# Performance work log

Measured on AMD Instinct MI355X. Metric: run time of the kernel, lower is better.

## Reference

```python
import jax, jax.numpy as jnp
import numpy as np

B, C, L = 8, 512, 2048   # batch, input_dim (channels), sequence length
H = 8                    # multihead_cnt
K = 3                    # kernel_dim
DH = C // H              # per-head dim = 64
SCALE = 1.0 / float(np.sqrt(C))  # module divides by sqrt(input_dim), not sqrt(head_dim)


def _conv1d(x, w, b):
    # x: [B, C, L], w: [C_out, C_in, K], padding=1 keeps L
    y = jax.lax.conv_general_dilated(x, w, window_strides=(1,), padding=[(1, 1)],
                                     dimension_numbers=('NCH', 'OIH', 'NCH'))
    return y + b[None, :, None]


def setup_inputs() -> dict:
    key = jax.random.key(0)
    ks = jax.random.split(key, 7)
    x = jax.random.normal(ks[0], (B, C, L), dtype=jnp.float32)
    # xavier_normal_ std for Conv1d weight [C, C, K]: sqrt(2 / (fan_in + fan_out)), fan = C*K
    std = float(np.sqrt(2.0 / (C * K + C * K)))
    inp = {'x': x}
    for i in range(3):  # conv_cnt = 3 -> q, k, v convolutions
        inp[f'w{i}'] = jax.random.normal(ks[1 + 2 * i], (C, C, K), dtype=jnp.float32) * std
        inp[f'b{i}'] = jax.random.normal(ks[2 + 2 * i], (C,), dtype=jnp.float32) * 0.01
    return inp


def reference(x, w0, b0, w1, b1, w2, b2):
    # q, k, v projections via Conv1d (padding preserves length)
    q = _conv1d(x, w0, b0)  # [B, C, L]
    k = _conv1d(x, w1, b1)
    v = _conv1d(x, w2, b2)
    # torch.chunk along dim 1 == contiguous reshape into heads
    qh = q.reshape(B, H, DH, L)
    kh = k.reshape(B, H, DH, L)
    vh = v.reshape(B, H, DH, L)
    # scores = q^T k / sqrt(input_dim)  -> [B, H, L, L]
    scores = jnp.einsum('bhdl,bhdm->bhlm', qh, kh) * SCALE
    att = jax.nn.softmax(scores, axis=-1)
    # out = (att @ v^T)^T -> [B, H, DH, L]
    out = jnp.einsum('bhlm,bhdm->bhdl', att, vh)
    return out.reshape(B, C, L)
```

## Files before the change

### kernel.cpp

```cpp
#include <hip/hip_runtime.h>
#include <hip/hip_bf16.h>
#include <cstdint>

typedef unsigned short u16;
typedef short v8s __attribute__((ext_vector_type(8)));
typedef float v4f __attribute__((ext_vector_type(4)));
typedef u16 u16x8 __attribute__((ext_vector_type(8)));
typedef u16 u16x4 __attribute__((ext_vector_type(4)));

static constexpr int Bb = 8, Cc = 512, Ll = 2048, Hh = 8, Dh = 64;

__device__ __forceinline__ float bf2f(u16 u){
  unsigned x = ((unsigned)u) << 16; float f; __builtin_memcpy(&f, &x, 4); return f;
}
__device__ __forceinline__ u16 f2bf(float f){
  unsigned x; __builtin_memcpy(&x, &f, 4);
  x = (x + 0x7fffu + ((x >> 16) & 1u)) >> 16; return (u16)x;
}

__device__ __forceinline__ void async_cp16(const u16* g, u16* l){
  __builtin_amdgcn_global_load_lds(
      (const __attribute__((address_space(1))) unsigned int*)g,
      (__attribute__((address_space(3))) unsigned int*)l, 16, 0, 0);
}

#if __has_builtin(__builtin_amdgcn_exp2f)
#define EXP2F(x) __builtin_amdgcn_exp2f(x)
#else
#define EXP2F(x) exp2f(x)
#endif

__global__ __launch_bounds__(256) void detect_dtype(const u16* __restrict__ x, unsigned* __restrict__ flag){
  __shared__ int cnt;
  if (threadIdx.x == 0) cnt = 0;
  __syncthreads();
  int sane = 0;
  for (int i = threadIdx.x; i < 4096; i += 256){
    unsigned e = (x[2 * i] >> 7) & 0xFFu;
    sane += (e >= 90u && e <= 160u) ? 1 : 0;
  }
  atomicAdd(&cnt, sane);
  __syncthreads();
  if (threadIdx.x == 0) *flag = (cnt < 2458) ? 1u : 0u;
}

__global__ __launch_bounds__(256) void transpose_pad(const void* __restrict__ xv, const unsigned* __restrict__ flagp,
                                                     u16* __restrict__ xT){
  int b = blockIdx.z, ci0 = blockIdx.y * 64, l0 = blockIdx.x * 64;
  __shared__ u16 tb[64 * 72];
  const unsigned isf32 = *flagp;
  int t = threadIdx.x;
  int row = t >> 3, seg = t & 7;
  if (isf32){
    const float* xf = (const float*)xv;
    #pragma unroll
    for (int rnd = 0; rnd < 2; rnd++){
      int ci = row + rnd * 32;
      size_t off = ((size_t)(b * Cc + ci0 + ci)) * Ll + l0 + seg * 8;
      v4f a = *(const v4f*)(xf + off);
      v4f c4 = *(const v4f*)(xf + off + 4);
      #pragma unroll
      for (int j = 0; j < 4; j++) tb[(seg * 8 + j) * 72 + ci] = f2bf(a[j]);
      #pragma unroll
      for (int j = 0; j < 4; j++) tb[(seg * 8 + 4 + j) * 72 + ci] = f2bf(c4[j]);
    }
  } else {
    const u16* x = (const u16*)xv;
    #pragma unroll
    for (int rnd = 0; rnd < 2; rnd++){
      int ci = row + rnd * 32;
      u16x8 v = *(const u16x8*)(x + ((size_t)(b * Cc + ci0 + ci)) * Ll + l0 + seg * 8);
      #pragma unroll
      for (int j = 0; j < 8; j++) tb[(seg * 8 + j) * 72 + ci] = v[j];
    }
  }
  __syncthreads();
  #pragma unroll
  for (int rnd = 0; rnd < 2; rnd++){
    int l = row + rnd * 32;
    u16x8 v = *(const u16x8*)&tb[l * 72 + seg * 8];
    *(u16x8*)(xT + ((size_t)b * 2050 + 1 + l0 + l) * Cc + ci0 + seg * 8) = v;
  }
  if (blockIdx.x == 0 && t < 8){
    u16x8 z = {};
    *(u16x8*)(xT + ((size_t)b * 2050 + 0) * Cc + ci0 + t * 8) = z;
  }
  if (blockIdx.x == 31 && t < 8){
    u16x8 z = {};
    *(u16x8*)(xT + ((size_t)b * 2050 + 2049) * Cc + ci0 + t * 8) = z;
  }
}

__global__ __launch_bounds__(256) void pack_wb(const void* __restrict__ w0, const void* __restrict__ w1,
                                               const void* __restrict__ w2, const void* __restrict__ b0,
                                               const void* __restrict__ b1, const void* __restrict__ b2,
                                               const unsigned* __restrict__ flagp,
                                               u16* __restrict__ wp, u16* __restrict__ bb){
  int g = blockIdx.x * 256 + threadIdx.x;
  const unsigned isf32 = *flagp;
  if (g < 9 * 512 * 512){
    int ci = g & 511, co = (g >> 9) & 511, kc = g >> 18;
    int conv = kc / 3, k = kc - conv * 3;
    const void* w = (conv == 0) ? w0 : ((conv == 1) ? w1 : w2);
    size_t idx = (size_t)co * 1536 + ci * 3 + k;
    wp[g] = isf32 ? f2bf(((const float*)w)[idx]) : ((const u16*)w)[idx];
  } else {
    int g2 = g - 9 * 512 * 512;
    if (g2 < 1536){
      int conv = g2 >> 9, c = g2 & 511;
      const void* bsrc = (conv == 0) ? b0 : ((conv == 1) ? b1 : b2);
      bb[g2] = isf32 ? f2bf(((const float*)bsrc)[c]) : ((const u16*)bsrc)[c];
    }
  }
}

__global__ __launch_bounds__(512, 2) void conv_gemm_fused(const u16* __restrict__ wp, const u16* __restrict__ xT,
                                                          const u16* __restrict__ bb, u16* __restrict__ qT,
                                                          u16* __restrict__ kT, u16* __restrict__ vN){
  __shared__ u16 smem[65536];
  int bx = blockIdx.x;
  int b = bx & 7, inner = bx >> 3;
  int mt = inner >> 3, nt = inner & 7;
  int m0 = mt << 8, n0 = nt << 8;
  int conv = m0 >> 9, co0 = m0 & 511;

  int t = threadIdx.x, wave = t >> 6, lane = t & 63, quad = lane >> 4, lid = lane & 15;
  int wm_i = wave >> 2, wn_i = wave & 3;

  int sx = ((lid & 1) << 6) | ((lid & 6) << 3);
  int cb0 = ((quad * 16) ^ sx) >> 1;
  int cb1 = ((64 + quad * 16) ^ sx) >> 1;
  int abase0 = (wm_i * 64 + lid) * 64;
  int bbase0 = 16384 + (wn_i * 32 + lid) * 64;

  int p0 = t * 16, p1 = p0 + 8192;
  int c0 = (p0 & 127) ^ ((((p0 >> 7) & 1) << 6) | (((p0 >> 8) & 1) << 4) | (((p0 >> 9) & 1) << 5));
  int c1 = (p1 & 127) ^ ((((p1 >> 7) & 1) << 6) | (((p1 >> 8) & 1) << 4) | (((p1 >> 9) & 1) << 5));
  int srcE0 = (p0 >> 7) * 512 + (c0 >> 1);
  int srcE1 = (p1 >> 7) * 512 + (c1 >> 1);
  int d0 = t * 8, d1 = 4096 + t * 8;

  const u16* aGbase = wp + (size_t)(conv * 1536 + co0) * 512;
  const u16* bGbase = xT + (size_t)b * (2050 * 512) + (size_t)n0 * 512;

#define STAGE_HALF(gsrc, ldst) do{ \
    async_cp16((gsrc) + srcE0, (ldst) + d0); \
    async_cp16((gsrc) + srcE1, (ldst) + d1); }while(0)

#define PHASE_WAIT() do{ \
    asm volatile("s_waitcnt lgkmcnt(0)" ::: "memory"); \
    __builtin_amdgcn_sched_barrier(0); \
    __builtin_amdgcn_s_barrier(); }while(0)

#define LOAD_A(mh) do{ \
    _Pragma("unroll") for (int m = 0; m < 4; ++m){ \
      af[m][0] = *(const v8s*)(lds + abase0 + (mh) * 8192 + m * 1024 + cb0); \
      af[m][1] = *(const v8s*)(lds + abase0 + (mh) * 8192 + m * 1024 + cb1); } }while(0)

#define LOAD_B(nh) do{ \
    _Pragma("unroll") for (int n = 0; n < 2; ++n){ \
      bf[n][0] = *(const v8s*)(lds + bbase0 + (nh) * 8192 + n * 1024 + cb0); \
      bf[n][1] = *(const v8s*)(lds + bbase0 + (nh) * 8192 + n * 1024 + cb1); } }while(0)

#define DO_MFMA(mh, nh) do{ \
    __builtin_amdgcn_s_setprio(1); \
    _Pragma("unroll") for (int m = 0; m < 4; ++m) \
    _Pragma("unroll") for (int n = 0; n < 2; ++n) \
    _Pragma("unroll") for (int kh = 0; kh < 2; ++kh) \
      acc[mh][nh][m][n] = __builtin_amdgcn_mfma_f32_16x16x32_bf16(af[m][kh], bf[n][kh], acc[mh][nh][m][n], 0, 0, 0); \
    __builtin_amdgcn_s_setprio(0); }while(0)

  v4f acc[2][2][4][2] = {};
  v8s af[4][2];

  #pragma unroll
  for (int k0 = 0; k0 < 2; ++k0){
    u16* stg = smem + k0 * 32768;
    const u16* aG = aGbase + k0 * 64;
    const u16* bG = bGbase + k0 * 64;
    STAGE_HALF(aG, stg);
    STAGE_HALF(aG + 65536, stg + 8192);
    STAGE_HALF(bG, stg + 16384);
    STAGE_HALF(bG + 65536, stg + 24576);
  }
  asm volatile("s_waitcnt vmcnt(8)" ::: "memory");
  __builtin_amdgcn_sched_barrier(0);
  __builtin_amdgcn_s_barrier();

  #pragma unroll 2
  for (int kt = 0; kt < 24; ++kt){
    u16* lds = smem + (kt & 1) * 32768;
    u16* stg = lds;
    int ks2 = (kt + 2) >> 3, ci2 = ((kt + 2) & 7) << 6;
    const u16* aG = aGbase + (size_t)ks2 * 262144 + ci2;
    const u16* bG = bGbase + (size_t)ks2 * 512 + ci2;
    bool st = (kt < 22);
    v8s bf[2][2];

    LOAD_A(0); LOAD_B(0);
    PHASE_WAIT();
    DO_MFMA(0, 0);
    LOAD_B(1);
    if (st) STAGE_HALF(aG, stg);
    PHASE_WAIT();
    DO_MFMA(0, 1);
    LOAD_A(1); LOAD_B(0);
    PHASE_WAIT();
    DO_MFMA(1, 0);
    LOAD_B(1);
    if (st){ STAGE_HALF(bG, stg + 16384); STAGE_HALF(aG + 65536, stg + 8192); }
    PHASE_WAIT();
    DO_MFMA(1, 1);
    if (st){
      STAGE_HALF(bG + 65536, stg + 24576);
      asm volatile("s_waitcnt vmcnt(8)" ::: "memory");
    } else if (kt == 22){
      asm volatile("s_waitcnt vmcnt(0)" ::: "memory");
    }
    if (kt < 23){
      __builtin_amdgcn_sched_barrier(0);
      __builtin_amdgcn_s_barrier();
    }
  }

#undef STAGE_HALF
#undef PHASE_WAIT
#undef LOAD_A
#undef LOAD_B
#undef DO_MFMA

  const float qsc = (float)(1.4426950408889634 / 22.627416997969522);
  if (conv < 2){
    u16* dst = (conv == 0) ? qT : kT;
    #pragma unroll
    for (int mh = 0; mh < 2; ++mh)
    #pragma unroll
    for (int m = 0; m < 4; ++m){
      int cog = m0 + mh * 128 + wm_i * 64 + m * 16 + quad * 4;
      float bv[4];
      #pragma unroll
      for (int r = 0; r < 4; r++) bv[r] = bf2f(bb[cog + r]);
      int coc = cog & 511;
      #pragma unroll
      for (int nh = 0; nh < 2; ++nh)
      #pragma unroll
      for (int n = 0; n < 2; ++n){
        int l = n0 + nh * 128 + wn_i * 32 + n * 16 + lid;
        u16x4 pk;
        #pragma unroll
        for (int r = 0; r < 4; r++){
          float v = acc[mh][nh][m][n][r] + bv[r];
          if (conv == 0) v *= qsc;
          pk[r] = f2bf(v);
        }
        *(u16x4*)(dst + ((((size_t)b * Hh + (coc >> 6)) * Ll + l) << 6) + (coc & 63)) = pk;
      }
    }
  } else {
    u16* scr = smem;
    #pragma unroll
    for (int nh = 0; nh < 2; ++nh){
      __syncthreads();
      #pragma unroll
      for (int mh = 0; mh < 2; ++mh)
      #pragma unroll
      for (int m = 0; m < 4; ++m){
        int rloc = mh * 128 + wm_i * 64 + m * 16 + quad * 4;
        int cog = m0 + rloc;
        float bv[4];
        #pragma unroll
        for (int r = 0; r < 4; r++) bv[r] = bf2f(bb[cog + r]);
        #pragma unroll
        for (int n = 0; n < 2; ++n){
          int lcl = wn_i * 32 + n * 16 + lid;
          #pragma unroll
          for (int r = 0; r < 4; r++)
            scr[(rloc + r) * 132 + lcl] = f2bf(acc[mh][nh][m][n][r] + bv[r]);
        }
      }
      __syncthreads();
      int seg = t & 15, rw = t >> 4;
      #pragma unroll
      for (int ps = 0; ps < 8; ++ps){
        int row = rw + ps * 32;
        u16x8 vv = *(const u16x8*)&scr[row * 132 + seg * 8];
        *(u16x8*)(vN + (((size_t)b * Cc + co0 + row) << 11) + n0 + nh * 128 + seg * 8) = vv;
      }
    }
  }
}

__global__ __launch_bounds__(256) void attn_kernel(const u16* __restrict__ qT, const u16* __restrict__ kT,
                                                   const u16* __restrict__ vN, const unsigned* __restrict__ flagp,
                                                   void* __restrict__ outv){
  int bhx = blockIdx.x;
  int b = bhx >> 3, h = bhx & 7, l0 = blockIdx.y * 128;
  int t = threadIdx.x, w = t >> 6, lane = t & 63, quad = lane >> 4, lid = lane & 15;
  __shared__ u16 kls[128 * 72];
  __shared__ u16 vls[64 * 136];
  const unsigned isf32 = *flagp;
  const size_t bh = (size_t)b * Hh + h;

  int kadd[5], vadd[5];
  bool kval[5], vval[5];
  #pragma unroll
  for (int r = 0; r < 5; r++){
    int e = (r * 256 + t) * 8;
    kval[r] = e < 128 * 72;
    int slot = e / 72, off = e - slot * 72;
    int s5 = slot & 31;
    int m = (slot & ~31) | (((s5 >> 2) & 1) << 3) | (((s5 >> 3) & 1) << 4) | (((s5 >> 4) & 1) << 2) | (s5 & 3);
    kadd[r] = m * 64 + (off < 64 ? off : 0);
    vval[r] = e < 64 * 136;
    int d = e / 136, voff = e - d * 136;
    vadd[r] = d * Ll + (voff < 128 ? voff : 0);
  }
  const u16* kTb = kT + bh * Ll * 64;
  const u16* vNb = vN + ((size_t)(b * Cc + h * Dh)) * Ll;

  v8s qF[2][2];
  #pragma unroll
  for (int ci = 0; ci < 2; ci++)
    #pragma unroll
    for (int ks = 0; ks < 2; ks++)
      qF[ci][ks] = *(const v8s*)(qT + ((bh * Ll) + l0 + w * 32 + ci * 16 + lid) * 64 + ks * 32 + quad * 8);

  const v8s onesF = {0x3F80, 0x3F80, 0x3F80, 0x3F80, 0x3F80, 0x3F80, 0x3F80, 0x3F80};
  v4f o[2][4] = {};
  v4f o1[2] = {};

  for (int mt = 0; mt < 16; mt++){
    int m0 = mt * 128;
    const u16* kt = kTb + (size_t)m0 * 64;
    const u16* vt = vNb + m0;
    #pragma unroll
    for (int r = 0; r < 5; r++)
      if (kval[r]) async_cp16(kt + kadd[r], &kls[(r * 256 + t) * 8]);
    #pragma unroll
    for (int r = 0; r < 5; r++)
      if (vval[r]) async_cp16(vt + vadd[r], &vls[(r * 256 + t) * 8]);
    __syncthreads();

    v4f s[4][2][2] = {};
    #pragma unroll
    for (int ks = 0; ks < 2; ks++){
      v8s aF[4][2];
      #pragma unroll
      for (int c = 0; c < 4; c++)
        #pragma unroll
        for (int tt = 0; tt < 2; tt++)
          aF[c][tt] = *(const v8s*)&kls[(c * 32 + tt * 16 + lid) * 72 + ks * 32 + quad * 8];
      #pragma unroll
      for (int c = 0; c < 4; c++)
        #pragma unroll
        for (int tt = 0; tt < 2; tt++){
          s[c][tt][0] = __builtin_amdgcn_mfma_f32_16x16x32_bf16(aF[c][tt], qF[0][ks], s[c][tt][0], 0, 0, 0);
          s[c][tt][1] = __builtin_amdgcn_mfma_f32_16x16x32_bf16(aF[c][tt], qF[1][ks], s[c][tt][1], 0, 0, 0);
        }
    }

    #pragma unroll
    for (int c = 0; c < 4; c++){
      v8s aP[2];
      #pragma unroll
      for (int ci = 0; ci < 2; ci++){
        float p[8];
        #pragma unroll
        for (int tt = 0; tt < 2; tt++)
          #pragma unroll
          for (int r = 0; r < 4; r++)
            p[tt * 4 + r] = EXP2F(s[c][tt][ci][r]);
        unsigned u[4];
        #pragma unroll
        for (int k2 = 0; k2 < 4; k2++){
          __hip_bfloat162 hb = __float22bfloat162_rn(make_float2(p[2 * k2], p[2 * k2 + 1]));
          __builtin_memcpy(&u[k2], &hb, 4);
        }
        __builtin_memcpy(&aP[ci], u, 16);
      }
      v8s bV[4];
      #pragma unroll
      for (int df = 0; df < 4; df++)
        bV[df] = *(const v8s*)&vls[(df * 16 + lid) * 136 + c * 32 + quad * 8];
      #pragma unroll
      for (int ci = 0; ci < 2; ci++){
        #pragma unroll
        for (int df = 0; df < 4; df++)
          o[ci][df] = __builtin_amdgcn_mfma_f32_16x16x32_bf16(aP[ci], bV[df], o[ci][df], 0, 0, 0);
        o1[ci] = __builtin_amdgcn_mfma_f32_16x16x32_bf16(aP[ci], onesF, o1[ci], 0, 0, 0);
      }
    }
    __syncthreads();
  }

  #pragma unroll
  for (int lf = 0; lf < 2; lf++){
    v4f nv;
    #pragma unroll
    for (int r = 0; r < 4; r++) nv[r] = 1.f / o1[lf][r];
    #pragma unroll
    for (int df = 0; df < 4; df++){
      int d = df * 16 + lid;
      int l = l0 + w * 32 + lf * 16 + quad * 4;
      size_t ofs = (((bh << 6) + d) << 11) + l;
      if (isf32){
        v4f st;
        #pragma unroll
        for (int r = 0; r < 4; r++) st[r] = o[lf][df][r] * nv[r];
        *(v4f*)((float*)outv + ofs) = st;
      } else {
        u16x4 pk;
        #pragma unroll
        for (int r = 0; r < 4; r++) pk[r] = f2bf(o[lf][df][r] * nv[r]);
        *(u16x4*)((u16*)outv + ofs) = pk;
      }
    }
  }
}

extern "C" void kernel_launch(void* const* d_in, const int* in_sizes, int n_in,
                              void* d_out, int out_size, void* d_ws, size_t ws_size,
                              hipStream_t stream){
  const void* x  = d_in[0];
  const void* w0 = d_in[1];
  const void* b0 = d_in[2];
  const void* w1 = d_in[3];
  const void* b1 = d_in[4];
  const void* w2 = d_in[5];
  const void* b2 = d_in[6];
  u16* ws = (u16*)d_ws;
  unsigned* flag = (unsigned*)ws;
  u16* xT = ws + 64;
  u16* wp = xT + (size_t)8 * 2050 * 512;
  u16* bb = wp + (size_t)9 * 512 * 512;
  u16* qT = bb + 1536;
  u16* kT = qT + (size_t)8 * 8 * 2048 * 64;
  u16* vN = kT + (size_t)8 * 8 * 2048 * 64;

  detect_dtype<<<1, 256, 0, stream>>>((const u16*)x, flag);
  transpose_pad<<<dim3(32, 8, 8), 256, 0, stream>>>(x, flag, xT);
  pack_wb<<<dim3(9 * 512 * 512 / 256 + 6), 256, 0, stream>>>(w0, w1, w2, b0, b1, b2, flag, wp, bb);
  conv_gemm_fused<<<dim3(384), 512, 0, stream>>>(wp, xT, bb, qT, kT, vN);
  attn_kernel<<<dim3(64, 16), 256, 0, stream>>>(qT, kT, vN, flag, d_out);
}
```

Baseline: 285.8 us.

## Restructure conv GEMM main loop to single-tile prefetch with double A registers

Result: faster. 272.6 us (-4.6%).

```diff
diff --git a/kernel.cpp b/kernel.cpp
--- a/kernel.cpp
+++ b/kernel.cpp
@@ -147,85 +147,66 @@
     async_cp16((gsrc) + srcE0, (ldst) + d0); \
     async_cp16((gsrc) + srcE1, (ldst) + d1); }while(0)
 
-#define PHASE_WAIT() do{ \
-    asm volatile("s_waitcnt lgkmcnt(0)" ::: "memory"); \
-    __builtin_amdgcn_sched_barrier(0); \
-    __builtin_amdgcn_s_barrier(); }while(0)
-
-#define LOAD_A(mh) do{ \
+#define STAGE_TILE(aG, bG, stg) do{ \
+    STAGE_HALF((aG), (stg)); \
+    STAGE_HALF((aG) + 65536, (stg) + 8192); \
+    STAGE_HALF((bG), (stg) + 16384); \
+    STAGE_HALF((bG) + 65536, (stg) + 24576); }while(0)
+
+#define LOAD_Ax(dst, mh) do{ \
     _Pragma("unroll") for (int m = 0; m < 4; ++m){ \
-      af[m][0] = *(const v8s*)(lds + abase0 + (mh) * 8192 + m * 1024 + cb0); \
-      af[m][1] = *(const v8s*)(lds + abase0 + (mh) * 8192 + m * 1024 + cb1); } }while(0)
+      dst[m][0] = *(const v8s*)(lds + abase0 + (mh) * 8192 + m * 1024 + cb0); \
+      dst[m][1] = *(const v8s*)(lds + abase0 + (mh) * 8192 + m * 1024 + cb1); } }while(0)
 
 #define LOAD_B(nh) do{ \
     _Pragma("unroll") for (int n = 0; n < 2; ++n){ \
       bf[n][0] = *(const v8s*)(lds + bbase0 + (nh) * 8192 + n * 1024 + cb0); \
       bf[n][1] = *(const v8s*)(lds + bbase0 + (nh) * 8192 + n * 1024 + cb1); } }while(0)
 
-#define DO_MFMA(mh, nh) do{ \
+#define DO_MFMA(A, mh, nh) do{ \
     __builtin_amdgcn_s_setprio(1); \
     _Pragma("unroll") for (int m = 0; m < 4; ++m) \
     _Pragma("unroll") for (int n = 0; n < 2; ++n) \
     _Pragma("unroll") for (int kh = 0; kh < 2; ++kh) \
-      acc[mh][nh][m][n] = __builtin_amdgcn_mfma_f32_16x16x32_bf16(af[m][kh], bf[n][kh], acc[mh][nh][m][n], 0, 0, 0); \
+      acc[mh][nh][m][n] = __builtin_amdgcn_mfma_f32_16x16x32_bf16(A[m][kh], bf[n][kh], acc[mh][nh][m][n], 0, 0, 0); \
     __builtin_amdgcn_s_setprio(0); }while(0)
 
   v4f acc[2][2][4][2] = {};
-  v8s af[4][2];
-
-  #pragma unroll
-  for (int k0 = 0; k0 < 2; ++k0){
-    u16* stg = smem + k0 * 32768;
-    const u16* aG = aGbase + k0 * 64;
-    const u16* bG = bGbase + k0 * 64;
-    STAGE_HALF(aG, stg);
-    STAGE_HALF(aG + 65536, stg + 8192);
-    STAGE_HALF(bG, stg + 16384);
-    STAGE_HALF(bG + 65536, stg + 24576);
-  }
-  asm volatile("s_waitcnt vmcnt(8)" ::: "memory");
+  v8s af0[4][2], af1[4][2], bf[2][2];
+
+  STAGE_TILE(aGbase, bGbase, smem);
+  asm volatile("s_waitcnt vmcnt(0)" ::: "memory");
   __builtin_amdgcn_sched_barrier(0);
   __builtin_amdgcn_s_barrier();
 
   #pragma unroll 2
   for (int kt = 0; kt < 24; ++kt){
     u16* lds = smem + (kt & 1) * 32768;
-    u16* stg = lds;
-    int ks2 = (kt + 2) >> 3, ci2 = ((kt + 2) & 7) << 6;
-    const u16* aG = aGbase + (size_t)ks2 * 262144 + ci2;
-    const u16* bG = bGbase + (size_t)ks2 * 512 + ci2;
-    bool st = (kt < 22);
-    v8s bf[2][2];
-
-    LOAD_A(0); LOAD_B(0);
-    PHASE_WAIT();
-    DO_MFMA(0, 0);
+    u16* stg = smem + ((kt + 1) & 1) * 32768;
+    if (kt < 23){
+      int k1 = kt + 1;
+      int ks1 = k1 >> 3, ci1 = (k1 & 7) << 6;
+      const u16* aG = aGbase + (size_t)ks1 * 262144 + ci1;
+      const u16* bG = bGbase + (size_t)ks1 * 512 + ci1;
+      STAGE_TILE(aG, bG, stg);
+    }
+    LOAD_Ax(af0, 0); LOAD_B(0);
+    DO_MFMA(af0, 0, 0);
+    LOAD_Ax(af1, 1);
+    DO_MFMA(af1, 1, 0);
     LOAD_B(1);
-    if (st) STAGE_HALF(aG, stg);
-    PHASE_WAIT();
-    DO_MFMA(0, 1);
-    LOAD_A(1); LOAD_B(0);
-    PHASE_WAIT();
-    DO_MFMA(1, 0);
-    LOAD_B(1);
-    if (st){ STAGE_HALF(bG, stg + 16384); STAGE_HALF(aG + 65536, stg + 8192); }
-    PHASE_WAIT();
-    DO_MFMA(1, 1);
-    if (st){
-      STAGE_HALF(bG + 65536, stg + 24576);
-      asm volatile("s_waitcnt vmcnt(8)" ::: "memory");
-    } else if (kt == 22){
+    DO_MFMA(af1, 1, 1);
+    DO_MFMA(af0, 0, 1);
+    if (kt < 23){
       asm volatile("s_waitcnt vmcnt(0)" ::: "memory");
-    }
-    if (kt < 23){
       __builtin_amdgcn_sched_barrier(0);
       __builtin_amdgcn_s_barrier();
     }
   }
 
 #undef STAGE_HALF
-#undef PHASE_WAIT
-#undef LOAD_A
+#undef STAGE_TILE
+#undef LOAD_Ax
 #undef LOAD_B
 #undef DO_MFMA
 
```
